# Optimization experiments

Hardware: AMD Instinct MI355X
Metric: run time of the kernel (lower is better)

## Reference

```python
import jax, jax.numpy as jnp
import numpy as np

B, T, C, E = 2, 100, 80, 32
MH = MW = 64
IN_H = IN_W = 640.0
IOU_FACTOR, CLS_FACTOR, TOPK = 6.0, 0.5, 10
EPS = 1e-9


def get_anchors_and_scalers(fmaps, in_h, in_w):
    anchors, scalers = [], []
    for fh, fw in fmaps:
        stride = in_h / fh
        ys = (np.arange(fh) + 0.5) * stride
        xs = (np.arange(fw) + 0.5) * stride
        gy, gx = np.meshgrid(ys, xs, indexing='ij')
        anchors.append(np.stack([gx, gy], -1).reshape(-1, 2))
        scalers.append(np.full(fh * fw, stride))
    return (np.concatenate(anchors).astype(np.float32),
            np.concatenate(scalers).astype(np.float32))


def setup_inputs() -> dict:
    key = jax.random.key(0)
    ks = jax.random.split(key, 8)
    anchors_np, scalers_np = get_anchors_and_scalers([(80, 80), (40, 40), (20, 20)], IN_H, IN_W)
    anchors = jnp.asarray(anchors_np)
    scalers = jnp.asarray(scalers_np)
    A = anchors.shape[0]
    cls_logits = jax.random.normal(ks[0], (B, A, C), jnp.float32)
    wh = jax.random.uniform(ks[1], (B, A, 2), jnp.float32, 16.0, 160.0)
    ctr = anchors[None] + jax.random.normal(ks[2], (B, A, 2), jnp.float32) * 8.0
    pred_boxes = jnp.clip(jnp.concatenate([ctr - wh / 2, ctr + wh / 2], -1), 0.0, IN_W)
    mask_embs = jax.random.normal(ks[3], (B, A, E), jnp.float32)
    protos = jax.random.normal(ks[4], (B, MH, MW, E), jnp.float32)
    tl = jax.random.uniform(ks[5], (B, T, 2), jnp.float32, 0.0, 560.0)
    twh = jax.random.uniform(ks[6], (B, T, 2), jnp.float32, 30.0, 240.0)
    target_bbox = jnp.concatenate([tl, jnp.minimum(tl + twh, IN_W)], -1)
    target_cls = jax.random.randint(ks[7], (B, T), 0, C, jnp.int32)
    target_masks = (jax.random.uniform(jax.random.fold_in(key, 7), (B, MH, MW, T)) > 0.5).astype(jnp.float32)
    return {'cls_logits': cls_logits, 'pred_boxes': pred_boxes, 'mask_embs': mask_embs,
            'protos': protos, 'target_cls': target_cls, 'target_bbox': target_bbox,
            'target_masks': target_masks, 'anchors': anchors, 'scalers': scalers}


def _ciou_pairwise(gt, pr):
    # gt [B,T,4], pr [B,A,4] -> [B,T,A]
    g = gt[:, :, None, :]
    p = pr[:, None, :, :]
    ix1 = jnp.maximum(g[..., 0], p[..., 0]); iy1 = jnp.maximum(g[..., 1], p[..., 1])
    ix2 = jnp.minimum(g[..., 2], p[..., 2]); iy2 = jnp.minimum(g[..., 3], p[..., 3])
    inter = jnp.clip(ix2 - ix1, 0.0) * jnp.clip(iy2 - iy1, 0.0)
    wg = g[..., 2] - g[..., 0]; hg = g[..., 3] - g[..., 1]
    wp = p[..., 2] - p[..., 0]; hp = p[..., 3] - p[..., 1]
    union = wg * hg + wp * hp - inter + EPS
    iou = inter / union
    cw = jnp.maximum(g[..., 2], p[..., 2]) - jnp.minimum(g[..., 0], p[..., 0])
    ch = jnp.maximum(g[..., 3], p[..., 3]) - jnp.minimum(g[..., 1], p[..., 1])
    c2 = cw * cw + ch * ch + EPS
    rho2 = ((g[..., 0] + g[..., 2] - p[..., 0] - p[..., 2]) ** 2 +
            (g[..., 1] + g[..., 3] - p[..., 1] - p[..., 3]) ** 2) / 4.0
    v = (4.0 / (jnp.pi ** 2)) * (jnp.arctan(wg / (hg + EPS)) - jnp.arctan(wp / (hp + EPS))) ** 2
    alpha = jax.lax.stop_gradient(v / (1.0 - iou + v + EPS))
    return iou - rho2 / c2 - alpha * v


def _bbox_mask(boxes, mh, mw, in_h, in_w):
    # boxes [B,A,4] pixel xyxy -> [B,A,mh,mw] binary inside-box mask on mask grid
    sx, sy = mw / in_w, mh / in_h
    x1, y1, x2, y2 = boxes[..., 0] * sx, boxes[..., 1] * sy, boxes[..., 2] * sx, boxes[..., 3] * sy
    rows = jnp.arange(mh, dtype=boxes.dtype)
    cols = jnp.arange(mw, dtype=boxes.dtype)
    rm = (rows >= y1[..., None]) & (rows < y2[..., None])  # [B,A,mh]
    cm = (cols >= x1[..., None]) & (cols < x2[..., None])  # [B,A,mw]
    return (rm[..., :, None] & cm[..., None, :]).astype(boxes.dtype)


def _assign_and_build(cls_logits, pred_boxes, mask_embs, protos,
                      target_cls, target_bbox, target_masks, anchors, scalers):
    Bn, A, Cn = cls_logits.shape
    mh, mw = protos.shape[1], protos.shape[2]
    # --- task-aligned assigner ---
    lt, rb = target_bbox[:, :, None, :2], target_bbox[:, :, None, 2:]
    deltas = jnp.concatenate([anchors[None, None] - lt, rb - anchors[None, None]], -1)
    grid_mask = (jnp.min(deltas, -1) > 0).astype(cls_logits.dtype)  # [B,T,A]
    iou_mat = jnp.clip(_ciou_pairwise(target_bbox, pred_boxes), 0.0, 1.0)  # [B,T,A]
    cls_prob = jax.nn.sigmoid(cls_logits)  # [B,A,C]
    oh_t = jax.nn.one_hot(target_cls, Cn, dtype=cls_prob.dtype)  # [B,T,C]
    cls_mat = jnp.einsum('btc,bac->bta', oh_t, cls_prob)  # [B,T,A]
    tmat = grid_mask * (iou_mat ** IOU_FACTOR) * (cls_mat ** CLS_FACTOR)
    kth = jax.lax.top_k(tmat, TOPK)[0][..., -1:]  # [B,T,1]
    topk_targets = jnp.where((tmat >= kth) & (tmat > 0), tmat, 0.0)
    unique_idx = jnp.argmax(topk_targets, axis=1)  # [B,A] best GT per anchor
    valid = (jnp.sum(topk_targets, axis=1) > 0).astype(cls_logits.dtype)  # [B,A]
    align_bbox = jnp.take_along_axis(target_bbox, jnp.broadcast_to(unique_idx[..., None], (Bn, A, 4)), axis=1)
    align_cls_idx = jnp.take_along_axis(target_cls, unique_idx, axis=1)  # [B,A]
    max_target = jnp.max(tmat, axis=-1, keepdims=True)
    max_iou = jnp.max(iou_mat, axis=-1, keepdims=True)
    norm_term = tmat / (max_target + EPS) * max_iou  # [B,T,A]
    norm_g = jnp.take_along_axis(jnp.transpose(norm_term, (0, 2, 1)), unique_idx[..., None], axis=2)  # [B,A,1]
    align_cls = jax.nn.one_hot(align_cls_idx, Cn, dtype=cls_logits.dtype) * norm_g * valid[..., None]
    # --- loss-target assembly (compute_loss body) ---
    align_bbox_scaled = align_bbox / scalers[None, :, None]
    boxes_scaled = pred_boxes / scalers[None, :, None]
    box_target = jnp.concatenate([align_bbox_scaled, valid[..., None], align_cls], -1)
    box_mask = _bbox_mask(align_bbox, mh, mw, IN_H, IN_W)  # [B,A,mh,mw]
    valid_seg = box_mask * valid[..., None, None]
    seg_pred = jax.nn.sigmoid(jnp.einsum('bne,bhwe->bnhw', mask_embs, protos)) * valid_seg
    seg_pred = seg_pred.reshape(Bn, A, mh * mw)
    masks_t = jnp.transpose(target_masks, (0, 3, 1, 2))  # [B,T,mh,mw]
    idx4 = jnp.broadcast_to(unique_idx[..., None, None], (Bn, A, mh, mw))
    align_seg = (jnp.take_along_axis(masks_t, idx4, axis=1) * valid_seg).reshape(Bn, A, mh * mw)
    area = ((align_bbox[..., 2] - align_bbox[..., 0]) * (align_bbox[..., 3] - align_bbox[..., 1])
            / (IN_W * IN_H))
    seg_target = jnp.concatenate([area[..., None], valid[..., None], align_seg], -1)
    return jnp.concatenate([boxes_scaled, cls_logits, box_target, seg_pred, seg_target], -1)


def reference(cls_logits, pred_boxes, mask_embs, protos, target_cls, target_bbox,
              target_masks, anchors, scalers):
    return _assign_and_build(cls_logits, pred_boxes, mask_embs, protos,
                             target_cls, target_bbox, target_masks, anchors, scalers)
```

## Files before the change

kernel.cpp:

```cpp
#include <hip/hip_runtime.h>
#include <math.h>

#define A_TOT 8400
#define B_N   2
#define T_N   100
#define C_N   80
#define E_N   32
#define MH_N  64
#define MW_N  64
#define ROW_N 8363
#define NROWS (B_N*A_TOT)
#define EPSF  1e-9f
#define COMP_CAP 1536
#define NEGINF -1e30f
#define GOUT  2100

typedef float vfloat4 __attribute__((ext_vector_type(4)));

__device__ __forceinline__ float2 tmat_eval(
    float gx1, float gy1, float gx2, float gy2,
    float ax,  float ay,
    float px1, float py1, float px2, float py2,
    float cl, float atg, float atp) {
  float ix1 = fmaxf(gx1,px1), iy1 = fmaxf(gy1,py1);
  float ix2 = fminf(gx2,px2), iy2 = fminf(gy2,py2);
  float inter = fmaxf(ix2-ix1,0.f) * fmaxf(iy2-iy1,0.f);
  float wg = gx2-gx1, hg = gy2-gy1, wp = px2-px1, hp = py2-py1;
  float uni = wg*hg + wp*hp - inter + EPSF;
  float iou = inter / uni;
  float cw = fmaxf(gx2,px2) - fminf(gx1,px1);
  float ch = fmaxf(gy2,py2) - fminf(gy1,py1);
  float c2 = cw*cw + ch*ch + EPSF;
  float dx = gx1+gx2-px1-px2, dy = gy1+gy2-py1-py2;
  float rho2 = (dx*dx + dy*dy) * 0.25f;
  float da = atg - atp;
  float v  = 0.4052847345693511f * da * da;
  float alpha = v / (1.f - iou + v + EPSF);
  float ciou = iou - rho2/c2 - alpha*v;
  float iouc = fminf(fmaxf(ciou, 0.f), 1.f);

  float tm = 0.f;
  if (ax > gx1 && ay > gy1 && ax < gx2 && ay < gy2) {
    float cp = 1.f / (1.f + expf(-cl));
    float i2 = iouc * iouc;
    tm = i2*i2*i2 * sqrtf(cp);
  }
  return make_float2(tm, iouc);
}

__global__ __launch_bounds__(512) void k_score(
    const float* __restrict__ cls_logits, const float* __restrict__ pred_boxes,
    const float* __restrict__ target_bbox, const int* __restrict__ target_cls,
    const float* __restrict__ anchors,
    float* __restrict__ tmatT,
    float* __restrict__ kth, float* __restrict__ maxt, float* __restrict__ maxiou) {
  int bt   = blockIdx.x;
  int b    = bt / T_N;
  int t    = bt - b*T_N;
  int tid  = threadIdx.x;
  int lane = tid & 63, wid = tid >> 6;
  __shared__ float comp[COMP_CAP];
  __shared__ float redm[8], redi[8];
  __shared__ float wtop[8][10];
  __shared__ int   cnt;
  if (tid == 0) cnt = 0;
  __syncthreads();

  float4 g  = *(const float4*)(target_bbox + bt*4);
  int    tc = target_cls[bt];
  float atg = atanf((g.z - g.x) / ((g.w - g.y) + EPSF));

  float lm = 0.f, li = 0.f;
  for (int a = tid; a < A_TOT; a += 512) {
    float ax = anchors[a*2+0], ay = anchors[a*2+1];
    float4 pb = *(const float4*)(pred_boxes + ((size_t)(b*A_TOT+a))*4);
    float cl = cls_logits[((size_t)(b*A_TOT+a))*C_N + tc];
    float atp = atanf((pb.z - pb.x) / ((pb.w - pb.y) + EPSF));
    float2 r = tmat_eval(g.x,g.y,g.z,g.w, ax,ay, pb.x,pb.y,pb.z,pb.w,
                         cl, atg, atp);
    tmatT[((size_t)b*A_TOT + a)*T_N + t] = r.x;
    li = fmaxf(li, r.y);
    if (r.x > 0.f) {
      lm = fmaxf(lm, r.x);
      comp[atomicAdd(&cnt, 1)] = r.x;
    }
  }
  #pragma unroll
  for (int off = 32; off; off >>= 1) {
    lm = fmaxf(lm, __shfl_xor(lm, off));
    li = fmaxf(li, __shfl_xor(li, off));
  }
  if (lane == 0) { redm[wid] = lm; redi[wid] = li; }
  __syncthreads();
  if (tid == 0) {
    float m = redm[0], mi = redi[0];
    #pragma unroll
    for (int w = 1; w < 8; w++) { m = fmaxf(m, redm[w]); mi = fmaxf(mi, redi[w]); }
    maxt[bt] = m; maxiou[bt] = mi;
  }
  int count = cnt;

  int base = wid*64 + lane;
  float e0 = (base        < count) ? comp[base]        : NEGINF;
  float e1 = (base + 512  < count) ? comp[base + 512]  : NEGINF;
  float e2 = (base + 1024 < count) ? comp[base + 1024] : NEGINF;
  float mytop = NEGINF;
  #pragma unroll
  for (int k = 0; k < 10; k++) {
    float bv = e0; int bs = 0;
    if (e1 > bv) { bv = e1; bs = 1; }
    if (e2 > bv) { bv = e2; bs = 2; }
    float v = bv; int id = (lane << 2) | bs;
    #pragma unroll
    for (int off = 32; off; off >>= 1) {
      float ov = __shfl_xor(v, off); int oid = __shfl_xor(id, off);
      if (ov > v || (ov == v && oid < id)) { v = ov; id = oid; }
    }
    if ((id >> 2) == lane) {
      int s = id & 3;
      if (s == 0) e0 = NEGINF; else if (s == 1) e1 = NEGINF; else e2 = NEGINF;
    }
    if (lane == k) mytop = v;
  }
  if (lane < 10) wtop[wid][lane] = mytop;
  __syncthreads();

  if (wid == 0) {
    int ia = lane, ib = 64 + lane;
    float f0 = wtop[ia/10][ia%10];
    float f1 = (ib < 80) ? wtop[ib/10][ib%10] : NEGINF;
    float cur = NEGINF;
    #pragma unroll
    for (int k = 0; k < 10; k++) {
      float bv = f0; int bs = 0;
      if (f1 > bv) { bv = f1; bs = 1; }
      float v = bv; int id = (lane << 1) | bs;
      #pragma unroll
      for (int off = 32; off; off >>= 1) {
        float ov = __shfl_xor(v, off); int oid = __shfl_xor(id, off);
        if (ov > v || (ov == v && oid < id)) { v = ov; id = oid; }
      }
      if ((id >> 1) == lane) { if ((id & 1) == 0) f0 = NEGINF; else f1 = NEGINF; }
      cur = v;
    }
    if (lane == 0) kth[bt] = fmaxf(cur, 0.f);
  }
}

__global__ __launch_bounds__(256) void k_out(
    const float* __restrict__ cls_logits, const float* __restrict__ pred_boxes,
    const float* __restrict__ mask_embs,  const float* __restrict__ protos,
    const float* __restrict__ t_masks,    const float* __restrict__ tmatT,
    const float* __restrict__ kth, const float* __restrict__ maxt,
    const float* __restrict__ maxiou, const float* __restrict__ target_bbox,
    const int* __restrict__ target_cls, const float* __restrict__ scalers,
    float* __restrict__ out) {
  int lane = threadIdx.x & 63;
  int wid  = threadIdx.x >> 6;
  __shared__ float semb_s[4][E_N];
  unsigned wg = blockIdx.x * 4u + (unsigned)wid;

  for (unsigned row = wg; row < (unsigned)NROWS; row += GOUT*4u) {
    int b = row >= (unsigned)A_TOT;
    int a = (int)row - b*A_TOT;

    const float* trow = tmatT + (size_t)row * T_N;
    float v1 = 0.f; int t1 = 0x7fff;
    {
      float va = (lane < T_N) ? trow[lane] : 0.f;
      if (lane < T_N && va > 0.f && va >= kth[b*T_N + lane]) { v1 = va; t1 = lane; }
      int l2 = lane + 64;
      if (l2 < T_N) {
        float vb = trow[l2];
        if (vb > 0.f && vb >= kth[b*T_N + l2]) {
          if (vb > v1) { v1 = vb; t1 = l2; }
        }
      }
    }
    #pragma unroll
    for (int off = 32; off; off >>= 1) {
      float ov = __shfl_xor(v1, off); int ot = __shfl_xor(t1, off);
      if (ov > v1 || (ov == v1 && ot < t1)) { v1 = ov; t1 = ot; }
    }
    int  anyv = v1 > 0.f;
    int  u    = anyv ? t1 : 0;
    int  bu   = b*T_N + u;
    float4 tb = *(const float4*)(target_bbox + bu*4);
    float ng  = anyv ? v1 / (maxt[bu] + EPSF) * maxiou[bu] : 0.f;
    float vld = anyv ? 1.f : 0.f;
    float s   = scalers[a];
    float area = (tb.z - tb.x)*(tb.w - tb.y)/(640.f*640.f);
    int  ct   = target_cls[bu];
    bool valid = anyv != 0;
    size_t base = (size_t)row * ROW_N;

    if (lane < E_N) semb_s[wid][lane] = mask_embs[(size_t)row*E_N + lane];

    {
      unsigned p = (unsigned)lane;
      float val = (p < 4u) ? pred_boxes[(size_t)row*4 + p] / s
                           : cls_logits[(size_t)row*C_N + (p-4u)];
      out[base + p] = val;
    }
    if (lane < 28) {
      unsigned p = 64u + (unsigned)lane;
      if (p < 84u)       out[base + p] = cls_logits[(size_t)row*C_N + (p-4u)];
      else if (p < 88u) {
        float t = (p==84u)?tb.x:((p==85u)?tb.y:((p==86u)?tb.z:tb.w));
        out[base + p] = t / s;
      }
      else if (p == 88u) out[base + 88] = vld;
      else if (p == 89u) { if (valid) out[base + 89 + ct] = ng; }
      else if (p == 90u) out[base + 4265] = area;
      else               out[base + 4266] = vld;
    }

    if (valid) {
      float x1s=tb.x*0.1f, y1s=tb.y*0.1f, x2s=tb.z*0.1f, y2s=tb.w*0.1f;
      int hlo = max(0, (int)ceilf(y1s)), hhi = min(MH_N, (int)ceilf(y2s));
      int wlo = max(0, (int)ceilf(x1s)), whi = min(MW_N, (int)ceilf(x2s));
      int nw = whi - wlo, nh = hhi - hlo;
      int ncell = (nw > 0 && nh > 0) ? nw * nh : 0;
      for (int i = lane; i < ncell; i += 64) {
        int h = hlo + i / nw, w = wlo + i % nw;
        const float* pr = protos + ((size_t)((b*MH_N + h)*MW_N + w)) * E_N;
        float acc = 0.f;
        #pragma unroll
        for (int e = 0; e < E_N; e++) acc += semb_s[wid][e] * pr[e];
        int p = (h << 6) | w;
        out[base + 169  + p] = 1.f / (1.f + expf(-acc));
        out[base + 4267 + p] = t_masks[((size_t)((b*MH_N + h)*MW_N + w)) * T_N + u];
      }
    }
  }
}

extern "C" void kernel_launch(void* const* d_in, const int* in_sizes, int n_in,
                              void* d_out, int out_size, void* d_ws, size_t ws_size,
                              hipStream_t stream) {
  const float* cls_logits   = (const float*)d_in[0];
  const float* pred_boxes   = (const float*)d_in[1];
  const float* mask_embs    = (const float*)d_in[2];
  const float* protos       = (const float*)d_in[3];
  const int*   target_cls   = (const int*)  d_in[4];
  const float* target_bbox  = (const float*)d_in[5];
  const float* target_masks = (const float*)d_in[6];
  const float* anchors      = (const float*)d_in[7];
  const float* scalers      = (const float*)d_in[8];
  float* out = (float*)d_out;

  float* ws     = (float*)d_ws;
  float* tmatT  = ws;
  float* kth    = tmatT + (size_t)NROWS*T_N;
  float* maxt   = kth + B_N*T_N;
  float* maxiou = maxt + B_N*T_N;

  hipMemsetAsync(out, 0, (size_t)out_size * sizeof(float), stream);
  k_score<<<B_N*T_N, 512, 0, stream>>>(cls_logits, pred_boxes, target_bbox,
                                       target_cls, anchors, tmatT, kth, maxt, maxiou);
  k_out<<<GOUT, 256, 0, stream>>>(cls_logits, pred_boxes, mask_embs, protos,
                                  target_masks, tmatT, kth, maxt, maxiou,
                                  target_bbox, target_cls, scalers, out);
}
```

Baseline: 170.7 us.

## Transpose target masks and move box/logit copies into scoring kernel

The scoring kernel gains extra blocks. Some of them transpose target_masks from [B,H,W,T] to [B,T,H,W] so the output kernel reads mask rows contiguously instead of with a stride of T. Other extra blocks write the predicted-box and class-logit columns of the output, which takes that work out of k_out and lets it run beside the scoring blocks. This costs an extra workspace buffer and a full transpose pass over the masks.

```diff
diff --git a/kernel.cpp b/kernel.cpp
--- a/kernel.cpp
+++ b/kernel.cpp
@@ -13,6 +13,9 @@
 #define EPSF  1e-9f
 #define COMP_CAP 1536
 #define NEGINF -1e30f
+#define SCORE_B  200
+#define TRANS_E  216
+#define PREP_B   280
 #define GOUT  2100
 
 typedef float vfloat4 __attribute__((ext_vector_type(4)));
@@ -48,21 +51,57 @@
   return make_float2(tm, iouc);
 }
 
-__global__ __launch_bounds__(512) void k_score(
+__global__ __launch_bounds__(512) void k_prep(
     const float* __restrict__ cls_logits, const float* __restrict__ pred_boxes,
     const float* __restrict__ target_bbox, const int* __restrict__ target_cls,
-    const float* __restrict__ anchors,
-    float* __restrict__ tmatT,
-    float* __restrict__ kth, float* __restrict__ maxt, float* __restrict__ maxiou) {
-  int bt   = blockIdx.x;
-  int b    = bt / T_N;
-  int t    = bt - b*T_N;
+    const float* __restrict__ anchors, const float* __restrict__ scalers,
+    const float* __restrict__ t_masks,
+    float* __restrict__ tmatT, float* __restrict__ tmaskT,
+    float* __restrict__ kth, float* __restrict__ maxt, float* __restrict__ maxiou,
+    float* __restrict__ out) {
   int tid  = threadIdx.x;
   int lane = tid & 63, wid = tid >> 6;
+  unsigned bx = blockIdx.x;
   __shared__ float comp[COMP_CAP];
   __shared__ float redm[8], redi[8];
   __shared__ float wtop[8][10];
   __shared__ int   cnt;
+
+  if (bx >= PREP_B) return;
+  if (bx >= TRANS_E) {
+    unsigned wg = (bx - TRANS_E)*8u + (unsigned)wid;
+    for (unsigned row = wg; row < (unsigned)NROWS; row += 512u) {
+      int a = (int)(row >= (unsigned)A_TOT ? row - A_TOT : row);
+      float s = scalers[a];
+      size_t base = (size_t)row * ROW_N;
+      {
+        unsigned p = (unsigned)lane;
+        float val = (p < 4u) ? pred_boxes[(size_t)row*4 + p] / s
+                             : cls_logits[(size_t)row*C_N + (p-4u)];
+        out[base + p] = val;
+      }
+      if (lane < 20) {
+        unsigned p = 64u + (unsigned)lane;
+        out[base + p] = cls_logits[(size_t)row*C_N + (p-4u)];
+      }
+    }
+    return;
+  }
+  if (bx >= SCORE_B) {
+    int g = ((int)bx - SCORE_B)*512 + tid;
+    for (int task = g; task < B_N*T_N*MH_N; task += (TRANS_E-SCORE_B)*512) {
+      int b = task / (T_N*MH_N);
+      int r = task - b*T_N*MH_N;
+      int t = r / MH_N, h = r - t*MH_N;
+      const float* src = t_masks + ((size_t)((b*MH_N + h)*MW_N))*T_N + t;
+      float* dst = tmaskT + ((size_t)((b*T_N + t)*MH_N + h))*MW_N;
+      #pragma unroll 4
+      for (int w = 0; w < MW_N; w++) dst[w] = src[(size_t)w*T_N];
+    }
+    return;
+  }
+
+  int bt = (int)bx, b = bt / T_N, t = bt - b*T_N;
   if (tid == 0) cnt = 0;
   __syncthreads();
 
@@ -148,9 +187,8 @@
 }
 
 __global__ __launch_bounds__(256) void k_out(
-    const float* __restrict__ cls_logits, const float* __restrict__ pred_boxes,
     const float* __restrict__ mask_embs,  const float* __restrict__ protos,
-    const float* __restrict__ t_masks,    const float* __restrict__ tmatT,
+    const float* __restrict__ tmaskT,     const float* __restrict__ tmatT,
     const float* __restrict__ kth, const float* __restrict__ maxt,
     const float* __restrict__ maxiou, const float* __restrict__ target_bbox,
     const int* __restrict__ target_cls, const float* __restrict__ scalers,
@@ -196,23 +234,15 @@
 
     if (lane < E_N) semb_s[wid][lane] = mask_embs[(size_t)row*E_N + lane];
 
-    {
-      unsigned p = (unsigned)lane;
-      float val = (p < 4u) ? pred_boxes[(size_t)row*4 + p] / s
-                           : cls_logits[(size_t)row*C_N + (p-4u)];
-      out[base + p] = val;
-    }
-    if (lane < 28) {
-      unsigned p = 64u + (unsigned)lane;
-      if (p < 84u)       out[base + p] = cls_logits[(size_t)row*C_N + (p-4u)];
-      else if (p < 88u) {
-        float t = (p==84u)?tb.x:((p==85u)?tb.y:((p==86u)?tb.z:tb.w));
-        out[base + p] = t / s;
-      }
-      else if (p == 88u) out[base + 88] = vld;
-      else if (p == 89u) { if (valid) out[base + 89 + ct] = ng; }
-      else if (p == 90u) out[base + 4265] = area;
-      else               out[base + 4266] = vld;
+    if (lane < 8) {
+      if (lane < 4) {
+        float t = (lane==0)?tb.x:((lane==1)?tb.y:((lane==2)?tb.z:tb.w));
+        out[base + 84 + lane] = t / s;
+      }
+      else if (lane == 4) out[base + 88] = vld;
+      else if (lane == 5) { if (valid) out[base + 89 + ct] = ng; }
+      else if (lane == 6) out[base + 4265] = area;
+      else                out[base + 4266] = vld;
     }
 
     if (valid) {
@@ -221,6 +251,7 @@
       int wlo = max(0, (int)ceilf(x1s)), whi = min(MW_N, (int)ceilf(x2s));
       int nw = whi - wlo, nh = hhi - hlo;
       int ncell = (nw > 0 && nh > 0) ? nw * nh : 0;
+      const float* tmrow = tmaskT + (size_t)(b*T_N + u) * (MH_N*MW_N);
       for (int i = lane; i < ncell; i += 64) {
         int h = hlo + i / nw, w = wlo + i % nw;
         const float* pr = protos + ((size_t)((b*MH_N + h)*MW_N + w)) * E_N;
@@ -229,7 +260,7 @@
         for (int e = 0; e < E_N; e++) acc += semb_s[wid][e] * pr[e];
         int p = (h << 6) | w;
         out[base + 169  + p] = 1.f / (1.f + expf(-acc));
-        out[base + 4267 + p] = t_masks[((size_t)((b*MH_N + h)*MW_N + w)) * T_N + u];
+        out[base + 4267 + p] = tmrow[p];
       }
     }
   }
@@ -251,14 +282,16 @@
 
   float* ws     = (float*)d_ws;
   float* tmatT  = ws;
-  float* kth    = tmatT + (size_t)NROWS*T_N;
+  float* tmaskT = tmatT + (size_t)NROWS*T_N;
+  float* kth    = tmaskT + (size_t)B_N*T_N*MH_N*MW_N;
   float* maxt   = kth + B_N*T_N;
   float* maxiou = maxt + B_N*T_N;
 
   hipMemsetAsync(out, 0, (size_t)out_size * sizeof(float), stream);
-  k_score<<<B_N*T_N, 512, 0, stream>>>(cls_logits, pred_boxes, target_bbox,
-                                       target_cls, anchors, tmatT, kth, maxt, maxiou);
-  k_out<<<GOUT, 256, 0, stream>>>(cls_logits, pred_boxes, mask_embs, protos,
-                                  target_masks, tmatT, kth, maxt, maxiou,
-                                  target_bbox, target_cls, scalers, out);
-}
+  k_prep<<<PREP_B, 512, 0, stream>>>(cls_logits, pred_boxes, target_bbox,
+                                     target_cls, anchors, scalers, target_masks,
+                                     tmatT, tmaskT, kth, maxt, maxiou, out);
+  k_out<<<GOUT, 256, 0, stream>>>(mask_embs, protos, tmaskT, tmatT,
+                                  kth, maxt, maxiou, target_bbox,
+                                  target_cls, scalers, out);
+}
```

Result: slower. 211.8 us (+24.1%).

## Transpose target masks in extra prep blocks and double output grid

Applied to the files above, without the earlier changes.

Adds 256 extra blocks to the scoring kernel that transpose target_masks from [B,H,W,T] to [B,T,H,W] in workspace, running alongside the per-target scoring blocks. The output kernel then reads target masks contiguously per row instead of with a stride of T. The aim is to remove uncoalesced gathers in the mask-copy loop. The output grid is also doubled. The cost is an extra ~3.3MB read and write pass, plus workspace use.

```diff
diff --git a/kernel.cpp b/kernel.cpp
--- a/kernel.cpp
+++ b/kernel.cpp
@@ -13,7 +13,9 @@
 #define EPSF  1e-9f
 #define COMP_CAP 1536
 #define NEGINF -1e30f
-#define GOUT  2100
+#define SCORE_B  200
+#define PREP_B   456
+#define GOUT  4200
 
 typedef float vfloat4 __attribute__((ext_vector_type(4)));
 
@@ -48,21 +50,36 @@
   return make_float2(tm, iouc);
 }
 
-__global__ __launch_bounds__(512) void k_score(
+__global__ __launch_bounds__(512) void k_prep(
     const float* __restrict__ cls_logits, const float* __restrict__ pred_boxes,
     const float* __restrict__ target_bbox, const int* __restrict__ target_cls,
-    const float* __restrict__ anchors,
-    float* __restrict__ tmatT,
+    const float* __restrict__ anchors, const float* __restrict__ t_masks,
+    float* __restrict__ tmatT, float* __restrict__ tmaskT,
     float* __restrict__ kth, float* __restrict__ maxt, float* __restrict__ maxiou) {
-  int bt   = blockIdx.x;
-  int b    = bt / T_N;
-  int t    = bt - b*T_N;
   int tid  = threadIdx.x;
   int lane = tid & 63, wid = tid >> 6;
+  unsigned bx = blockIdx.x;
   __shared__ float comp[COMP_CAP];
   __shared__ float redm[8], redi[8];
   __shared__ float wtop[8][10];
   __shared__ int   cnt;
+
+  if (bx >= SCORE_B) {
+    const int NTH = (PREP_B - SCORE_B) * 512;
+    int g = ((int)bx - SCORE_B)*512 + tid;
+    const int TOT = B_N*T_N*MH_N*MW_N;
+    for (int i = g; i < TOT; i += NTH) {
+      float v = t_masks[i];
+      int t = i % T_N;
+      int r = i / T_N;
+      int w = r & 63, r2 = r >> 6;
+      int h = r2 & 63, b = r2 >> 6;
+      tmaskT[((size_t)((b*T_N + t)*MH_N + h))*MW_N + w] = v;
+    }
+    return;
+  }
+
+  int bt = (int)bx, b = bt / T_N, t = bt - b*T_N;
   if (tid == 0) cnt = 0;
   __syncthreads();
 
@@ -150,7 +167,7 @@
 __global__ __launch_bounds__(256) void k_out(
     const float* __restrict__ cls_logits, const float* __restrict__ pred_boxes,
     const float* __restrict__ mask_embs,  const float* __restrict__ protos,
-    const float* __restrict__ t_masks,    const float* __restrict__ tmatT,
+    const float* __restrict__ tmaskT,     const float* __restrict__ tmatT,
     const float* __restrict__ kth, const float* __restrict__ maxt,
     const float* __restrict__ maxiou, const float* __restrict__ target_bbox,
     const int* __restrict__ target_cls, const float* __restrict__ scalers,
@@ -221,6 +238,7 @@
       int wlo = max(0, (int)ceilf(x1s)), whi = min(MW_N, (int)ceilf(x2s));
       int nw = whi - wlo, nh = hhi - hlo;
       int ncell = (nw > 0 && nh > 0) ? nw * nh : 0;
+      const float* tmrow = tmaskT + (size_t)(b*T_N + u) * (MH_N*MW_N);
       for (int i = lane; i < ncell; i += 64) {
         int h = hlo + i / nw, w = wlo + i % nw;
         const float* pr = protos + ((size_t)((b*MH_N + h)*MW_N + w)) * E_N;
@@ -229,7 +247,7 @@
         for (int e = 0; e < E_N; e++) acc += semb_s[wid][e] * pr[e];
         int p = (h << 6) | w;
         out[base + 169  + p] = 1.f / (1.f + expf(-acc));
-        out[base + 4267 + p] = t_masks[((size_t)((b*MH_N + h)*MW_N + w)) * T_N + u];
+        out[base + 4267 + p] = tmrow[p];
       }
     }
   }
@@ -251,14 +269,16 @@
 
   float* ws     = (float*)d_ws;
   float* tmatT  = ws;
-  float* kth    = tmatT + (size_t)NROWS*T_N;
+  float* tmaskT = tmatT + (size_t)NROWS*T_N;
+  float* kth    = tmaskT + (size_t)B_N*T_N*MH_N*MW_N;
   float* maxt   = kth + B_N*T_N;
   float* maxiou = maxt + B_N*T_N;
 
   hipMemsetAsync(out, 0, (size_t)out_size * sizeof(float), stream);
-  k_score<<<B_N*T_N, 512, 0, stream>>>(cls_logits, pred_boxes, target_bbox,
-                                       target_cls, anchors, tmatT, kth, maxt, maxiou);
+  k_prep<<<PREP_B, 512, 0, stream>>>(cls_logits, pred_boxes, target_bbox,
+                                     target_cls, anchors, target_masks,
+                                     tmatT, tmaskT, kth, maxt, maxiou);
   k_out<<<GOUT, 256, 0, stream>>>(cls_logits, pred_boxes, mask_embs, protos,
-                                  target_masks, tmatT, kth, maxt, maxiou,
+                                  tmaskT, tmatT, kth, maxt, maxiou,
                                   target_bbox, target_cls, scalers, out);
 }
```

After: 173.8 us. Within noise of the previous version (+1.8%).
